# Kernel optimization log

Hardware: AMD Instinct MI355X
Metric: run time of the kernel (lower is better)

The kernel has to match this reference:

```python
import jax, jax.numpy as jnp
import numpy as np

B, N, D, H = 8, 2048, 1024, 1024

def setup_inputs() -> dict:
    key = jax.random.key(0)
    ks = jax.random.split(key, 7)
    s = 1.0 / np.sqrt(D)
    return {
        "x": jax.random.normal(ks[0], (B, N, D), dtype=jnp.float32),
        "Wq": jax.random.uniform(ks[1], (D, H), jnp.float32, -s, s),
        "bq": jax.random.uniform(ks[2], (H,), jnp.float32, -s, s),
        "Wk": jax.random.uniform(ks[3], (D, H), jnp.float32, -s, s),
        "bk": jax.random.uniform(ks[4], (H,), jnp.float32, -s, s),
        "Wv": jax.random.uniform(ks[5], (D, H), jnp.float32, -s, s),
        "bv": jax.random.uniform(ks[6], (H,), jnp.float32, -s, s),
    }

def reference(x, Wq, bq, Wk, bk, Wv, bv):
    # q, k, v: [B, N, H]
    q = jnp.einsum('bnd,dh->bnh', x, Wq) + bq
    k = jnp.einsum('bnd,dh->bnh', x, Wk) + bk
    v = jnp.einsum('bnd,dh->bnh', x, Wv) + bv
    scale = 1.0 / jnp.sqrt(jnp.asarray(q.shape[-1], q.dtype))
    score = jnp.einsum('bqh,bkh->bqk', q, k) * scale  # [B, N, N]
    causal = jnp.tril(jnp.ones((q.shape[1], q.shape[1]), dtype=bool))
    score = jnp.where(causal, score, -jnp.inf)
    attn = jax.nn.softmax(score, axis=-1)
    # dropout p=0.0 -> identity (deterministic reference)
    return jnp.einsum('bqk,bkh->bqh', attn, v)
```

## Files before the change

### kernel.cpp

```cpp
#include <hip/hip_runtime.h>
#include <hip/hip_bf16.h>
#include <stdint.h>

#define BB 8
#define NN 2048
#define DD 1024
#define HH 1024

using f32x4 = __attribute__((ext_vector_type(4))) float;
using s16x8 = __attribute__((ext_vector_type(8))) short;

__device__ __forceinline__ short f2bf(float f){
  union { float f; uint32_t u; } v; v.f = f;
  uint32_t r = (v.u + 0x7fffu + ((v.u >> 16) & 1u)) >> 16;
  return (short)r;
}
__device__ __forceinline__ float bf2f(short s){
  union { uint32_t u; float f; } v; v.u = ((uint32_t)(uint16_t)s) << 16; return v.f;
}

#define MFMA(a,b,c) __builtin_amdgcn_mfma_f32_16x16x32_bf16((a),(b),(c),0,0,0)

#define GL16(gp, lp) __builtin_amdgcn_global_load_lds( \
    (const __attribute__((address_space(1))) void*)(gp), \
    (__attribute__((address_space(3))) void*)(lp), 16, 0, 0)

__global__ __launch_bounds__(256) void k_conv_x(const float* __restrict__ x,
                                                short* __restrict__ xb){
  int gid = blockIdx.x*256 + threadIdx.x;
  const float4* xv = (const float4*)x;
  float4 a = xv[(size_t)gid*2], b2 = xv[(size_t)gid*2+1];
  s16x8 o;
  o[0]=f2bf(a.x);  o[1]=f2bf(a.y);  o[2]=f2bf(a.z);  o[3]=f2bf(a.w);
  o[4]=f2bf(b2.x); o[5]=f2bf(b2.y); o[6]=f2bf(b2.z); o[7]=f2bf(b2.w);
  *(s16x8*)(xb + (size_t)gid*8) = o;
}

__global__ __launch_bounds__(256) void k_conv_w(const float* __restrict__ Wq,
                                                const float* __restrict__ Wk,
                                                const float* __restrict__ Wv,
                                                short* __restrict__ Wt){
  __shared__ float tile[64][65];
  int bx = blockIdx.x; int mat = bx >> 8; int ti = bx & 255;
  int d0 = (ti >> 4) << 6, h0 = (ti & 15) << 6;
  const float* W = (mat==0) ? Wq : (mat==1 ? Wk : Wv);
  int t = threadIdx.x;
  for (int i=0;i<16;i++){ int e = i*256 + t; int r = e>>6, c = e&63;
    tile[r][c] = W[(size_t)(d0+r)*HH + h0 + c]; }
  __syncthreads();
  for (int i=0;i<16;i++){ int e = i*256 + t; int r = e>>6, c = e&63;
    Wt[(size_t)(mat*HH + h0 + r)*DD + d0 + c] = f2bf(tile[c][r]); }
}

__global__ __launch_bounds__(512,2) void k_gemm(const short* __restrict__ Aw,
                                                const short* __restrict__ Bw,
                                                const float* __restrict__ bq,
                                                const float* __restrict__ bk,
                                                const float* __restrict__ bv,
                                                short* __restrict__ Qw,
                                                short* __restrict__ Kw,
                                                short* __restrict__ Vw){
  __shared__ short Al[2][256*64];
  __shared__ short Bl[2][256*64];
  const int t = threadIdx.x, l = t & 63, w = t >> 6;
  const int g = l >> 4, c = l & 15;
  const int bid = blockIdx.x;
  const int bm = (bid & 7)*8 + ((bid >> 3) & 7);
  const int bn = bid >> 6;
  const int m0 = bm << 8, c0 = bn << 8;
  const int wr = w >> 2, wc = w & 3;
  f32x4 acc[8][4] = {};

  const int srow = l >> 3, schunk = l & 7;
  auto stageA = [&](int kt, int buf, int j){
    int row = j*64 + w*8 + srow;
    int u = schunk ^ (row & 7);
    GL16(Aw + (size_t)(m0+row)*DD + kt*64 + u*8,
         ((char*)&Al[buf][0]) + (j*64 + w*8)*128);
  };
  auto stageB = [&](int kt, int buf, int j){
    int row = j*64 + w*8 + srow;
    int u = schunk ^ (row & 7);
    GL16(Bw + (size_t)(c0+row)*DD + kt*64 + u*8,
         ((char*)&Bl[buf][0]) + (j*64 + w*8)*128);
  };

  #pragma unroll
  for (int j=0;j<4;j++){ stageA(0,0,j); stageB(0,0,j); }
  __syncthreads();

  for (int kt = 0; kt < 16; ++kt){
    const int cur = kt & 1;
    s16x8 bfr[4][2];
    #pragma unroll
    for (int ni=0;ni<4;ni++){
      int row = wc*64 + ni*16 + c;
      #pragma unroll
      for (int kk=0;kk<2;kk++)
        bfr[ni][kk] = *(const s16x8*)&Bl[cur][row*64 + (((kk*4+g)^(c&7))*8)];
    }
    #pragma unroll
    for (int h = 0; h < 2; ++h){
      s16x8 af[4][2];
      #pragma unroll
      for (int m2=0;m2<4;m2++){
        int row = wr*128 + (h*4+m2)*16 + c;
        #pragma unroll
        for (int kk=0;kk<2;kk++)
          af[m2][kk] = *(const s16x8*)&Al[cur][row*64 + (((kk*4+g)^(c&7))*8)];
      }
      if (h==0 && kt < 15){
        #pragma unroll
        for (int j=0;j<4;j++){ stageA(kt+1,cur^1,j); stageB(kt+1,cur^1,j); }
      }
      __builtin_amdgcn_s_barrier();
      __builtin_amdgcn_s_setprio(1);
      #pragma unroll
      for (int m2=0;m2<4;m2++)
        #pragma unroll
        for (int ni=0;ni<4;ni++)
          #pragma unroll
          for (int kk=0;kk<2;kk++)
            acc[h*4+m2][ni] = MFMA(bfr[ni][kk], af[m2][kk], acc[h*4+m2][ni]);
      __builtin_amdgcn_s_setprio(0);
      if (h==0) __builtin_amdgcn_s_barrier();
    }
    asm volatile("s_waitcnt vmcnt(0)" ::: "memory");
    __builtin_amdgcn_sched_barrier(0);
    __builtin_amdgcn_s_barrier();
  }

  const int mat = bn >> 2;
  short* Outp = (mat==0) ? Qw : (mat==1 ? Kw : Vw);
  const float* bias = (mat==0) ? bq : (mat==1 ? bk : bv);
  #pragma unroll
  for (int ni=0;ni<4;ni++){
    int col0 = (bn & 3)*256 + wc*64 + ni*16 + g*4;
    float4 bv4 = *(const float4*)&bias[col0];
    #pragma unroll
    for (int mi=0;mi<8;mi++){
      int orow = m0 + wr*128 + mi*16 + c;
      short4 pk;
      pk.x = f2bf(acc[mi][ni][0] + bv4.x);
      pk.y = f2bf(acc[mi][ni][1] + bv4.y);
      pk.z = f2bf(acc[mi][ni][2] + bv4.z);
      pk.w = f2bf(acc[mi][ni][3] + bv4.w);
      *(short4*)&Outp[(size_t)orow*HH + col0] = pk;
    }
  }
}

__global__ __launch_bounds__(256) void k_vtrans(const short* __restrict__ Vw,
                                                short* __restrict__ Vt){
  __shared__ uint16_t tile[64][65];
  int bx = blockIdx.x; int b = bx >> 9; int rem = bx & 511;
  int n0 = (rem >> 4) << 6, h0 = (rem & 15) << 6;
  int t = threadIdx.x;
  const uint16_t* vin = (const uint16_t*)Vw;
  uint16_t* vout = (uint16_t*)Vt;
  for (int i=0;i<16;i++){ int e = i*256 + t; int r = e>>6, c = e&63;
    tile[r][c] = vin[((size_t)b*NN + n0 + r)*HH + h0 + c]; }
  __syncthreads();
  for (int i=0;i<16;i++){ int e = i*256 + t; int r = e>>6, c = e&63;
    vout[((size_t)b*HH + h0 + r)*NN + n0 + c] = tile[c][r]; }
}

__global__ __launch_bounds__(256) void k_s(const short* __restrict__ Qw,
                                           const short* __restrict__ Kw,
                                           short* __restrict__ Pp){
  __shared__ short Ql[128*32];
  __shared__ short Kl[128*32];
  const int t = threadIdx.x, l = t & 63, w = t >> 6;
  const int g = l >> 4, c = l & 15;
  int p = blockIdx.x; int b = p & 7; int ti = p >> 3;
  int tr = 0; while ((tr+1)*(tr+2)/2 <= ti) tr++;
  int tc = ti - tr*(tr+1)/2;
  const short* Aq = Qw + ((size_t)b*NN + tr*128)*HH;
  const short* Bk = Kw + ((size_t)b*NN + tc*128)*HH;
  const float SC_EXP = 0.04508422002783268f;
  const int wq = w >> 1, wk = w & 1;
  f32x4 acc[4][4] = {};

  const int srow0 = w*32 + (l >> 2), srow1 = srow0 + 16;
  const int su0 = (l & 3) ^ ((srow0 >> 1) & 3);
  const int su1 = (l & 3) ^ ((srow1 >> 1) & 3);
  const short* Qs0 = Aq + (size_t)srow0*HH + su0*8;
  const short* Qs1 = Aq + (size_t)srow1*HH + su1*8;
  const short* Ks0 = Bk + (size_t)srow0*HH + su0*8;
  const short* Ks1 = Bk + (size_t)srow1*HH + su1*8;
  const int rchunk = (g ^ ((c>>1)&3)) * 8;
  int qoff[4], koff[4];
  #pragma unroll
  for (int mi=0;mi<4;mi++) qoff[mi] = (wq*64 + mi*16 + c)*32 + rchunk;
  #pragma unroll
  for (int ni=0;ni<4;ni++) koff[ni] = (wk*64 + ni*16 + c)*32 + rchunk;

  for (int kt = 0; kt < 32; ++kt){
    int ko = kt*32;
    __syncthreads();
    GL16(Qs0 + ko, (char*)&Ql[(w*32)*32]);
    GL16(Qs1 + ko, (char*)&Ql[(w*32+16)*32]);
    GL16(Ks0 + ko, (char*)&Kl[(w*32)*32]);
    GL16(Ks1 + ko, (char*)&Kl[(w*32+16)*32]);
    __syncthreads();
    s16x8 qf[4], kf[4];
    #pragma unroll
    for (int mi=0;mi<4;mi++) qf[mi] = *(const s16x8*)&Ql[qoff[mi]];
    #pragma unroll
    for (int ni=0;ni<4;ni++) kf[ni] = *(const s16x8*)&Kl[koff[ni]];
    #pragma unroll
    for (int mi=0;mi<4;mi++)
      #pragma unroll
      for (int ni=0;ni<4;ni++)
        acc[mi][ni] = MFMA(kf[ni], qf[mi], acc[mi][ni]);
  }

  short* Pt = Pp + ((size_t)b*136 + ti)*16384;
  #pragma unroll
  for (int ni=0;ni<4;ni++){
    int pc0 = wk*64 + ni*16 + g*4;
    #pragma unroll
    for (int mi=0;mi<4;mi++){
      int pr = wq*64 + mi*16 + c;
      short4 pk;
      #pragma unroll
      for (int i=0;i<4;i++){
        bool keep = (tc*128 + pc0 + i) <= (tr*128 + pr);
        float pv = keep ? exp2f(acc[mi][ni][i]*SC_EXP) : 0.f;
        ((short*)&pk)[i] = f2bf(pv);
      }
      *(short4*)&Pt[pr*128 + pc0] = pk;
    }
  }
}

__global__ __launch_bounds__(256) void k_pv(const short* __restrict__ Pp,
                                            const short* __restrict__ Vt,
                                            float* __restrict__ out){
  __shared__ short Pl[128*32];
  __shared__ short Vl[128*32];
  const int t = threadIdx.x, l = t & 63, w = t >> 6;
  const int g = l >> 4, c = l & 15;
  int p = blockIdx.x;
  int r = p >> 8, j = p & 255;
  int tr, id;
  if      (r==0){ tr = j>>4;        id = (j&15); }
  else if (r==1){ tr = 15-(j>>4);   id = 16 + (j&15); }
  else if (r==2){ tr = (j&15);      id = 32 + (j>>4); }
  else          { tr = 15-(j&15);   id = 48 + (j>>4); }
  int b = id & 7, hc = id >> 3;
  const short* Pb = Pp + ((size_t)b*136 + tr*(tr+1)/2)*16384;
  const short* Bv = Vt + ((size_t)b*HH + hc*128)*NN;
  const int wp = w >> 1, wh = w & 1;
  f32x4 acc[4][4] = {};
  float ls[4] = {0.f,0.f,0.f,0.f};

  const int srow0 = w*32 + (l >> 2), srow1 = srow0 + 16;
  const int su0 = (l & 3) ^ ((srow0 >> 1) & 3);
  const int su1 = (l & 3) ^ ((srow1 >> 1) & 3);
  const int rchunk = (g ^ ((c>>1)&3)) * 8;
  int poff[4], voff[4];
  #pragma unroll
  for (int mi=0;mi<4;mi++) poff[mi] = (wp*64 + mi*16 + c)*32 + rchunk;
  #pragma unroll
  for (int ni=0;ni<4;ni++) voff[ni] = (wh*64 + ni*16 + c)*32 + rchunk;

  const int nst = (tr+1)*4;
  for (int kt = 0; kt < nst; ++kt){
    const short* Ps = Pb + (size_t)(kt>>2)*16384 + (kt&3)*32;
    __syncthreads();
    GL16(Ps + srow0*128 + su0*8, (char*)&Pl[(w*32)*32]);
    GL16(Ps + srow1*128 + su1*8, (char*)&Pl[(w*32+16)*32]);
    GL16(Bv + (size_t)srow0*NN + kt*32 + su0*8, (char*)&Vl[(w*32)*32]);
    GL16(Bv + (size_t)srow1*NN + kt*32 + su1*8, (char*)&Vl[(w*32+16)*32]);
    __syncthreads();
    s16x8 pf[4], vf[4];
    #pragma unroll
    for (int mi=0;mi<4;mi++) pf[mi] = *(const s16x8*)&Pl[poff[mi]];
    #pragma unroll
    for (int ni=0;ni<4;ni++) vf[ni] = *(const s16x8*)&Vl[voff[ni]];
    #pragma unroll
    for (int mi=0;mi<4;mi++)
      #pragma unroll
      for (int e=0;e<8;e++) ls[mi] += bf2f(pf[mi][e]);
    #pragma unroll
    for (int mi=0;mi<4;mi++)
      #pragma unroll
      for (int ni=0;ni<4;ni++)
        acc[mi][ni] = MFMA(vf[ni], pf[mi], acc[mi][ni]);
  }
  #pragma unroll
  for (int mi=0;mi<4;mi++){
    ls[mi] += __shfl_xor(ls[mi], 16);
    ls[mi] += __shfl_xor(ls[mi], 32);
  }
  #pragma unroll
  for (int mi=0;mi<4;mi++){
    float linv = 1.0f / ls[mi];
    int orow = tr*128 + wp*64 + mi*16 + c;
    #pragma unroll
    for (int ni=0;ni<4;ni++){
      int h0 = hc*128 + wh*64 + ni*16 + g*4;
      float4 o4;
      o4.x = acc[mi][ni][0]*linv; o4.y = acc[mi][ni][1]*linv;
      o4.z = acc[mi][ni][2]*linv; o4.w = acc[mi][ni][3]*linv;
      *(float4*)&out[((size_t)(b*NN + orow))*HH + h0] = o4;
    }
  }
}

extern "C" void kernel_launch(void* const* d_in, const int* in_sizes, int n_in,
                              void* d_out, int out_size, void* d_ws, size_t ws_size,
                              hipStream_t stream) {
  const float* x  = (const float*)d_in[0];
  const float* Wq = (const float*)d_in[1];
  const float* bq = (const float*)d_in[2];
  const float* Wk = (const float*)d_in[3];
  const float* bk = (const float*)d_in[4];
  const float* Wv = (const float*)d_in[5];
  const float* bv = (const float*)d_in[6];
  char* ws = (char*)d_ws;
  short* xb = (short*)(ws);
  short* Pp = (short*)(ws);
  short* Wt = (short*)(ws + 35651584u);
  short* Qw = (short*)(ws + 41943040u);
  short* Kw = (short*)(ws + 75497472u);
  short* Vw = (short*)(ws + 109051904u);
  short* Vt = (short*)(ws + 142606336u);

  k_conv_x<<<8192, 256, 0, stream>>>(x, xb);
  k_conv_w<<<768, 256, 0, stream>>>(Wq, Wk, Wv, Wt);
  k_gemm<<<768, 512, 0, stream>>>(xb, Wt, bq, bk, bv, Qw, Kw, Vw);
  k_vtrans<<<4096, 256, 0, stream>>>(Vw, Vt);
  k_s<<<1088, 256, 0, stream>>>(Qw, Kw, Pp);
  k_pv<<<1024, 256, 0, stream>>>(Pp, Vt, (float*)d_out);
}
```

Measured before the change: 292.3 us.

## Restructure QKV GEMM into 4-stage K=32 LDS pipeline with counted vmcnt waits

Replaces the double-buffered K=64 tile loop in the QKV projection GEMM with a 4-slot ring of K=32 tiles, prefetching three stages ahead. Each iteration waits with vmcnt(8) instead of draining all outstanding loads, and uses one barrier per step. LDS swizzle offsets are precomputed once. The aim is to hide global-to-LDS latency better and cut barrier overhead, at the cost of more iterations with fewer MFMAs each and trickier wait-count correctness.

```diff
diff --git a/kernel.cpp b/kernel.cpp
--- a/kernel.cpp
+++ b/kernel.cpp
@@ -60,8 +60,8 @@
                                                 short* __restrict__ Qw,
                                                 short* __restrict__ Kw,
                                                 short* __restrict__ Vw){
-  __shared__ short Al[2][256*64];
-  __shared__ short Bl[2][256*64];
+  __shared__ short Al[4][256*32];
+  __shared__ short Bl[4][256*32];
   const int t = threadIdx.x, l = t & 63, w = t >> 6;
   const int g = l >> 4, c = l & 15;
   const int bid = blockIdx.x;
@@ -71,64 +71,65 @@
   const int wr = w >> 2, wc = w & 3;
   f32x4 acc[8][4] = {};
 
-  const int srow = l >> 3, schunk = l & 7;
-  auto stageA = [&](int kt, int buf, int j){
-    int row = j*64 + w*8 + srow;
-    int u = schunk ^ (row & 7);
-    GL16(Aw + (size_t)(m0+row)*DD + kt*64 + u*8,
-         ((char*)&Al[buf][0]) + (j*64 + w*8)*128);
+  const int sr = t >> 2, sch = t & 3;
+  const int u0 = sch ^ ((sr >> 1) & 3);
+  const int u1 = sch ^ (((sr + 128) >> 1) & 3);
+  const short* A0 = Aw + (size_t)(m0 + sr)*DD + u0*8;
+  const short* A1 = Aw + (size_t)(m0 + sr + 128)*DD + u1*8;
+  const short* B0 = Bw + (size_t)(c0 + sr)*DD + u0*8;
+  const short* B1 = Bw + (size_t)(c0 + sr + 128)*DD + u1*8;
+  const int d0b = sr*64 + sch*16, d1b = (sr+128)*64 + sch*16;
+  auto stage = [&](int kt){
+    int s = kt & 3, ko = kt*32;
+    GL16(A0 + ko, (char*)&Al[s][0] + d0b);
+    GL16(A1 + ko, (char*)&Al[s][0] + d1b);
+    GL16(B0 + ko, (char*)&Bl[s][0] + d0b);
+    GL16(B1 + ko, (char*)&Bl[s][0] + d1b);
   };
-  auto stageB = [&](int kt, int buf, int j){
-    int row = j*64 + w*8 + srow;
-    int u = schunk ^ (row & 7);
-    GL16(Bw + (size_t)(c0+row)*DD + kt*64 + u*8,
-         ((char*)&Bl[buf][0]) + (j*64 + w*8)*128);
-  };
-
-  #pragma unroll
-  for (int j=0;j<4;j++){ stageA(0,0,j); stageB(0,0,j); }
-  __syncthreads();
-
-  for (int kt = 0; kt < 16; ++kt){
-    const int cur = kt & 1;
-    s16x8 bfr[4][2];
-    #pragma unroll
-    for (int ni=0;ni<4;ni++){
-      int row = wc*64 + ni*16 + c;
-      #pragma unroll
-      for (int kk=0;kk<2;kk++)
-        bfr[ni][kk] = *(const s16x8*)&Bl[cur][row*64 + (((kk*4+g)^(c&7))*8)];
-    }
-    #pragma unroll
-    for (int h = 0; h < 2; ++h){
-      s16x8 af[4][2];
-      #pragma unroll
-      for (int m2=0;m2<4;m2++){
-        int row = wr*128 + (h*4+m2)*16 + c;
-        #pragma unroll
-        for (int kk=0;kk<2;kk++)
-          af[m2][kk] = *(const s16x8*)&Al[cur][row*64 + (((kk*4+g)^(c&7))*8)];
-      }
-      if (h==0 && kt < 15){
-        #pragma unroll
-        for (int j=0;j<4;j++){ stageA(kt+1,cur^1,j); stageB(kt+1,cur^1,j); }
-      }
-      __builtin_amdgcn_s_barrier();
-      __builtin_amdgcn_s_setprio(1);
-      #pragma unroll
-      for (int m2=0;m2<4;m2++)
-        #pragma unroll
-        for (int ni=0;ni<4;ni++)
-          #pragma unroll
-          for (int kk=0;kk<2;kk++)
-            acc[h*4+m2][ni] = MFMA(bfr[ni][kk], af[m2][kk], acc[h*4+m2][ni]);
-      __builtin_amdgcn_s_setprio(0);
-      if (h==0) __builtin_amdgcn_s_barrier();
-    }
-    asm volatile("s_waitcnt vmcnt(0)" ::: "memory");
+
+  int aoff[8], boff[4];
+  #pragma unroll
+  for (int mi=0;mi<8;mi++){
+    int row = wr*128 + mi*16 + c;
+    aoff[mi] = row*32 + (g ^ ((row>>1)&3))*8;
+  }
+  #pragma unroll
+  for (int ni=0;ni<4;ni++){
+    int row = wc*64 + ni*16 + c;
+    boff[ni] = row*32 + (g ^ ((row>>1)&3))*8;
+  }
+
+  auto body = [&](int kt, bool dostage){
+    int s = kt & 3;
     __builtin_amdgcn_sched_barrier(0);
     __builtin_amdgcn_s_barrier();
-  }
+    __builtin_amdgcn_sched_barrier(0);
+    s16x8 af[8], bfr[4];
+    #pragma unroll
+    for (int mi=0;mi<8;mi++) af[mi] = *(const s16x8*)&Al[s][aoff[mi]];
+    #pragma unroll
+    for (int ni=0;ni<4;ni++) bfr[ni] = *(const s16x8*)&Bl[s][boff[ni]];
+    if (dostage) stage(kt+3);
+    asm volatile("s_waitcnt lgkmcnt(0)" ::: "memory");
+    __builtin_amdgcn_sched_barrier(0);
+    __builtin_amdgcn_s_setprio(1);
+    #pragma unroll
+    for (int mi=0;mi<8;mi++)
+      #pragma unroll
+      for (int ni=0;ni<4;ni++)
+        acc[mi][ni] = MFMA(bfr[ni], af[mi], acc[mi][ni]);
+    __builtin_amdgcn_s_setprio(0);
+  };
+
+  stage(0); stage(1); stage(2);
+  for (int kt = 0; kt < 30; ++kt){
+    asm volatile("s_waitcnt vmcnt(8)" ::: "memory");
+    body(kt, kt < 29);
+  }
+  asm volatile("s_waitcnt vmcnt(4)" ::: "memory");
+  body(30, false);
+  asm volatile("s_waitcnt vmcnt(0)" ::: "memory");
+  body(31, false);
 
   const int mat = bn >> 2;
   short* Outp = (mat==0) ? Qw : (mat==1 ? Kw : Vw);
```

Measured after the change: 298.9 us. 1.02x slower.
